# Performance work log

Hardware: AMD Instinct MI355X
Metric: run time of the kernel (lower is better)

Reference implementation:

```python
import jax, jax.numpy as jnp
import numpy as np

D = 256

def setup_inputs() -> dict:
    key = jax.random.key(0)
    k1, k2, k3, k4, k5, k6 = jax.random.split(key, 6)
    M, N = 2048, 512
    s = 1.0 / np.sqrt(D)
    return {
        "q_vec": jax.random.normal(k1, (M, D), dtype=jnp.float32),
        "kv": jax.random.normal(k2, (M, N, D), dtype=jnp.float32),
        "wq": jax.random.uniform(k3, (D, D), jnp.float32, -s, s),
        "wk": jax.random.uniform(k4, (D, D), jnp.float32, -s, s),
        "wv": jax.random.uniform(k5, (D, D), jnp.float32, -s, s),
        "wo": (jax.random.uniform(k6, (D, D), jnp.float32, -s, s)),
    }

def reference(q_vec, kv, wq, wk, wv, wo):
    # q_vec: [M, d], kv: [M, N, d]; weights stored torch-style [out, in] -> apply x @ W.T
    d = q_vec.shape[-1]
    q = q_vec @ wq.T                          # [M, d]
    k = jnp.einsum('mnd,ed->mne', kv, wk)     # [M, N, d]
    v = jnp.einsum('mnd,ed->mne', kv, wv)     # [M, N, d]
    logits = jnp.einsum('md,mnd->mn', q, k) / jnp.sqrt(jnp.float32(d))  # [M, N]
    attn = jax.nn.softmax(logits, axis=-1)    # [M, N] (dropout p=0.0 is identity)
    ctx = jnp.einsum('mn,mnd->md', attn, v)   # [M, d]
    out = ctx @ wo.T                          # [M, d]
    return out, attn
```

## Files before the change

### kernel.cpp

```cpp
#include <hip/hip_runtime.h>
#include <math.h>

#define DD 256
#define MM 2048
#define NN 512

typedef float f32x4 __attribute__((ext_vector_type(4)));

__device__ inline f32x4 ld_nt(const f32x4* p) {
    return __builtin_nontemporal_load(p);
}

__global__ void prep_weights(const float* __restrict__ wq, const float* __restrict__ wk,
                             const float* __restrict__ wv, const float* __restrict__ wo,
                             float* __restrict__ B1, float* __restrict__ B2T) {
    __shared__ float sA[DD];
    const int j = threadIdx.x;
    const int b = blockIdx.x;
    if (b < DD) {
        const int d = b;
        sA[j] = wq[j * DD + d];
        __syncthreads();
        float acc = 0.f;
        for (int a = 0; a < DD; ++a) acc = fmaf(sA[a], wk[a * DD + j], acc);
        B1[d * DD + j] = acc * 0.0625f;
    } else {
        const int d = b - DD;
        sA[j] = wv[j * DD + d];
        __syncthreads();
        float acc = 0.f;
        for (int e = 0; e < DD; ++e) acc = fmaf(wo[j * DD + e], sA[e], acc);
        B2T[d * DD + j] = acc;
    }
}

__global__ __launch_bounds__(256, 4)
void attn_fused(const float* __restrict__ q_vec, const float* __restrict__ kv,
                const float* __restrict__ B1, const float* __restrict__ B2T,
                float* __restrict__ out, float* __restrict__ attn_out) {
    __shared__ float s_pe[NN];
    __shared__ float s_lw[4];
    __shared__ float s_wc[4][DD];
    __shared__ float s_q[DD];
    __shared__ float s_qt[DD];

    const int m    = blockIdx.x;
    const int tid  = threadIdx.x;
    const int wave = tid >> 6;
    const int lane = tid & 63;
    const int grp  = lane >> 4;
    const int l16  = lane & 15;

    s_q[tid] = q_vec[(size_t)m * DD + tid];
    __syncthreads();
    {
        float a = 0.f;
#pragma unroll 8
        for (int d = 0; d < DD; ++d) a = fmaf(s_q[d], B1[d * DD + tid], a);
        s_qt[tid] = a;
    }
    __syncthreads();

    const f32x4* qt4 = (const f32x4*)s_qt;
    const f32x4 qv0 = qt4[l16];
    const f32x4 qv1 = qt4[l16 + 16];
    const f32x4 qv2 = qt4[l16 + 32];
    const f32x4 qv3 = qt4[l16 + 48];

    const int nbase = wave * 4 + grp;
    const f32x4* p = (const f32x4*)(kv + (size_t)m * NN * DD) + (size_t)nbase * 64 + l16;
    const int STRIDE = 16 * 64;

    f32x4 c0 = (f32x4)0.f, c1 = (f32x4)0.f, c2 = (f32x4)0.f, c3 = (f32x4)0.f;
    float lw = 0.f;

    f32x4 a0 = ld_nt(p), a1 = ld_nt(p + 16), a2 = ld_nt(p + 32), a3 = ld_nt(p + 48);

#pragma unroll 2
    for (int it = 0; it < NN / 16; ++it) {
        f32x4 b0, b1, b2, b3;
        if (it + 1 < NN / 16) {
            const f32x4* np = p + (size_t)(it + 1) * STRIDE;
            b0 = ld_nt(np); b1 = ld_nt(np + 16); b2 = ld_nt(np + 32); b3 = ld_nt(np + 48);
        }
        f32x4 t = a0 * qv0 + a1 * qv1 + a2 * qv2 + a3 * qv3;
        float pdot = (t[0] + t[1]) + (t[2] + t[3]);
        pdot += __shfl_xor(pdot, 1);
        pdot += __shfl_xor(pdot, 2);
        pdot += __shfl_xor(pdot, 4);
        pdot += __shfl_xor(pdot, 8);

        const float pe = __expf(pdot);
        if (l16 == 0) s_pe[it * 16 + nbase] = pe;
        lw += pe;

        c0 += pe * a0;
        c1 += pe * a1;
        c2 += pe * a2;
        c3 += pe * a3;

        a0 = b0; a1 = b1; a2 = b2; a3 = b3;
    }

#pragma unroll
    for (int i = 0; i < 4; ++i) {
        c0[i] += __shfl_xor(c0[i], 16); c1[i] += __shfl_xor(c1[i], 16);
        c2[i] += __shfl_xor(c2[i], 16); c3[i] += __shfl_xor(c3[i], 16);
        c0[i] += __shfl_xor(c0[i], 32); c1[i] += __shfl_xor(c1[i], 32);
        c2[i] += __shfl_xor(c2[i], 32); c3[i] += __shfl_xor(c3[i], 32);
    }
    lw += __shfl_xor(lw, 16);
    lw += __shfl_xor(lw, 32);

    {
        f32x4* wc4 = (f32x4*)(&s_wc[wave][0]);
        const f32x4 cg = (grp == 0) ? c0 : (grp == 1) ? c1 : (grp == 2) ? c2 : c3;
        wc4[grp * 16 + l16] = cg;
        if (lane == 0) s_lw[wave] = lw;
    }
    __syncthreads();

    const float L = s_lw[0] + s_lw[1] + s_lw[2] + s_lw[3];
    const float invL = 1.f / L;

    float cd = (s_wc[0][tid] + s_wc[1][tid]) + (s_wc[2][tid] + s_wc[3][tid]);
    cd *= invL;
    __syncthreads();
    s_q[tid] = cd;
    __syncthreads();

    attn_out[(size_t)m * NN + tid]       = s_pe[tid] * invL;
    attn_out[(size_t)m * NN + tid + 256] = s_pe[tid + 256] * invL;

    float o = 0.f;
#pragma unroll 8
    for (int d = 0; d < DD; ++d) o = fmaf(s_q[d], B2T[d * DD + tid], o);
    out[(size_t)m * DD + tid] = o;
}

extern "C" void kernel_launch(void* const* d_in, const int* in_sizes, int n_in,
                              void* d_out, int out_size, void* d_ws, size_t ws_size,
                              hipStream_t stream) {
    const float* q_vec = (const float*)d_in[0];
    const float* kv    = (const float*)d_in[1];
    const float* wq    = (const float*)d_in[2];
    const float* wk    = (const float*)d_in[3];
    const float* wv    = (const float*)d_in[4];
    const float* wo    = (const float*)d_in[5];

    float* out  = (float*)d_out;
    float* attn = (float*)d_out + (size_t)MM * DD;

    float* B1  = (float*)d_ws;
    float* B2T = B1 + DD * DD;

    prep_weights<<<2 * DD, DD, 0, stream>>>(wq, wk, wv, wo, B1, B2T);
    attn_fused<<<MM, DD, 0, stream>>>(q_vec, kv, B1, B2T, out, attn);
}
```

Baseline: 208.8 us.

## Process two query rows per block with deeper kv prefetch and shared weight reads

Each block now handles two rows of M, so every weight element read in the query projection and the output projection serves two rows. The kv streaming loop now runs across both rows with a two-stage register prefetch, and the first kv tiles are issued before the projection so memory latency overlaps it. The grid is halved to 1024 blocks, leaving fewer blocks to hide latency, and the extra prefetch registers may reduce occupancy.

Measured after the change: 467.8 us. 124% more time.

```diff
diff --git a/kernel.cpp b/kernel.cpp
--- a/kernel.cpp
+++ b/kernel.cpp
@@ -7,13 +7,11 @@
 
 typedef float f32x4 __attribute__((ext_vector_type(4)));
 
-__device__ inline f32x4 ld_nt(const f32x4* p) {
-    return __builtin_nontemporal_load(p);
-}
+__device__ inline f32x4 ld_nt(const f32x4* p) { return __builtin_nontemporal_load(p); }
 
 __global__ void prep_weights(const float* __restrict__ wq, const float* __restrict__ wk,
                              const float* __restrict__ wv, const float* __restrict__ wo,
-                             float* __restrict__ B1, float* __restrict__ B2T) {
+                             float* __restrict__ W1, float* __restrict__ W2T) {
     __shared__ float sA[DD];
     const int j = threadIdx.x;
     const int b = blockIdx.x;
@@ -23,119 +21,139 @@
         __syncthreads();
         float acc = 0.f;
         for (int a = 0; a < DD; ++a) acc = fmaf(sA[a], wk[a * DD + j], acc);
-        B1[d * DD + j] = acc * 0.0625f;
+        W1[d * DD + j] = acc * 0.0625f;
     } else {
         const int d = b - DD;
         sA[j] = wv[j * DD + d];
         __syncthreads();
         float acc = 0.f;
         for (int e = 0; e < DD; ++e) acc = fmaf(wo[j * DD + e], sA[e], acc);
-        B2T[d * DD + j] = acc;
+        W2T[d * DD + j] = acc;
     }
 }
 
 __global__ __launch_bounds__(256, 4)
 void attn_fused(const float* __restrict__ q_vec, const float* __restrict__ kv,
-                const float* __restrict__ B1, const float* __restrict__ B2T,
+                const float* __restrict__ W1, const float* __restrict__ W2T,
                 float* __restrict__ out, float* __restrict__ attn_out) {
     __shared__ float s_pe[NN];
     __shared__ float s_lw[4];
     __shared__ float s_wc[4][DD];
-    __shared__ float s_q[DD];
-    __shared__ float s_qt[DD];
+    __shared__ float s_qa[DD], s_qb[DD];
+    __shared__ float s_qt0[DD], s_qt1[DD];
 
-    const int m    = blockIdx.x;
+    const int m0   = blockIdx.x * 2;
     const int tid  = threadIdx.x;
     const int wave = tid >> 6;
     const int lane = tid & 63;
     const int grp  = lane >> 4;
     const int l16  = lane & 15;
+    const int nbase = wave * 4 + grp;
 
-    s_q[tid] = q_vec[(size_t)m * DD + tid];
+    const f32x4* kvb = (const f32x4*)(kv + (size_t)m0 * NN * DD);
+    const int lofs   = nbase * 64 + l16;
+    const int STRIDE = 16 * 64;
+    const int NT     = 2 * NN / 16;
+
+    f32x4 A0, A1, A2, A3, P0, P1, P2, P3;
+    {
+        const f32x4* p = kvb + lofs;
+        A0 = ld_nt(p); A1 = ld_nt(p + 16); A2 = ld_nt(p + 32); A3 = ld_nt(p + 48);
+        const f32x4* q = kvb + STRIDE + lofs;
+        P0 = ld_nt(q); P1 = ld_nt(q + 16); P2 = ld_nt(q + 32); P3 = ld_nt(q + 48);
+    }
+
+    s_qa[tid] = q_vec[(size_t)m0 * DD + tid];
+    s_qb[tid] = q_vec[(size_t)m0 * DD + DD + tid];
     __syncthreads();
     {
-        float a = 0.f;
+        float t0 = 0.f, t1 = 0.f;
 #pragma unroll 8
-        for (int d = 0; d < DD; ++d) a = fmaf(s_q[d], B1[d * DD + tid], a);
-        s_qt[tid] = a;
+        for (int d = 0; d < DD; ++d) {
+            const float w = W1[d * DD + tid];
+            t0 = fmaf(s_qa[d], w, t0);
+            t1 = fmaf(s_qb[d], w, t1);
+        }
+        s_qt0[tid] = t0;
+        s_qt1[tid] = t1;
     }
     __syncthreads();
 
-    const f32x4* qt4 = (const f32x4*)s_qt;
-    const f32x4 qv0 = qt4[l16];
-    const f32x4 qv1 = qt4[l16 + 16];
-    const f32x4 qv2 = qt4[l16 + 32];
-    const f32x4 qv3 = qt4[l16 + 48];
+    for (int r = 0; r < 2; ++r) {
+        const f32x4* qt4 = (const f32x4*)(r == 0 ? s_qt0 : s_qt1);
+        const f32x4 qv0 = qt4[l16];
+        const f32x4 qv1 = qt4[l16 + 16];
+        const f32x4 qv2 = qt4[l16 + 32];
+        const f32x4 qv3 = qt4[l16 + 48];
 
-    const int nbase = wave * 4 + grp;
-    const f32x4* p = (const f32x4*)(kv + (size_t)m * NN * DD) + (size_t)nbase * 64 + l16;
-    const int STRIDE = 16 * 64;
+        f32x4 c0 = (f32x4)0.f, c1 = (f32x4)0.f, c2 = (f32x4)0.f, c3 = (f32x4)0.f;
+        float lw = 0.f;
 
-    f32x4 c0 = (f32x4)0.f, c1 = (f32x4)0.f, c2 = (f32x4)0.f, c3 = (f32x4)0.f;
-    float lw = 0.f;
+        for (int it = 0; it < NN / 16; ++it) {
+            const int g = r * (NN / 16) + it;
+            f32x4 N0, N1, N2, N3;
+            const bool pf = (g + 2 < NT);
+            if (pf) {
+                const f32x4* np = kvb + (size_t)(g + 2) * STRIDE + lofs;
+                N0 = ld_nt(np); N1 = ld_nt(np + 16); N2 = ld_nt(np + 32); N3 = ld_nt(np + 48);
+            }
 
-    f32x4 a0 = ld_nt(p), a1 = ld_nt(p + 16), a2 = ld_nt(p + 32), a3 = ld_nt(p + 48);
+            f32x4 t = A0 * qv0 + A1 * qv1 + A2 * qv2 + A3 * qv3;
+            float pd = (t[0] + t[1]) + (t[2] + t[3]);
+            pd += __shfl_xor(pd, 1);
+            pd += __shfl_xor(pd, 2);
+            pd += __shfl_xor(pd, 4);
+            pd += __shfl_xor(pd, 8);
 
-#pragma unroll 2
-    for (int it = 0; it < NN / 16; ++it) {
-        f32x4 b0, b1, b2, b3;
-        if (it + 1 < NN / 16) {
-            const f32x4* np = p + (size_t)(it + 1) * STRIDE;
-            b0 = ld_nt(np); b1 = ld_nt(np + 16); b2 = ld_nt(np + 32); b3 = ld_nt(np + 48);
+            const float pe = __expf(pd);
+            if (l16 == 0) s_pe[it * 16 + nbase] = pe;
+            lw += pe;
+
+            c0 += pe * A0; c1 += pe * A1; c2 += pe * A2; c3 += pe * A3;
+
+            A0 = P0; A1 = P1; A2 = P2; A3 = P3;
+            if (pf) { P0 = N0; P1 = N1; P2 = N2; P3 = N3; }
         }
-        f32x4 t = a0 * qv0 + a1 * qv1 + a2 * qv2 + a3 * qv3;
-        float pdot = (t[0] + t[1]) + (t[2] + t[3]);
-        pdot += __shfl_xor(pdot, 1);
-        pdot += __shfl_xor(pdot, 2);
-        pdot += __shfl_xor(pdot, 4);
-        pdot += __shfl_xor(pdot, 8);
 
-        const float pe = __expf(pdot);
-        if (l16 == 0) s_pe[it * 16 + nbase] = pe;
-        lw += pe;
+#pragma unroll
+        for (int i = 0; i < 4; ++i) {
+            c0[i] += __shfl_xor(c0[i], 16); c1[i] += __shfl_xor(c1[i], 16);
+            c2[i] += __shfl_xor(c2[i], 16); c3[i] += __shfl_xor(c3[i], 16);
+            c0[i] += __shfl_xor(c0[i], 32); c1[i] += __shfl_xor(c1[i], 32);
+            c2[i] += __shfl_xor(c2[i], 32); c3[i] += __shfl_xor(c3[i], 32);
+        }
+        lw += __shfl_xor(lw, 16);
+        lw += __shfl_xor(lw, 32);
 
-        c0 += pe * a0;
-        c1 += pe * a1;
-        c2 += pe * a2;
-        c3 += pe * a3;
+        {
+            f32x4* wc4 = (f32x4*)(&s_wc[wave][0]);
+            const f32x4 cg = (grp == 0) ? c0 : (grp == 1) ? c1 : (grp == 2) ? c2 : c3;
+            wc4[grp * 16 + l16] = cg;
+            if (lane == 0) s_lw[wave] = lw;
+        }
+        __syncthreads();
 
-        a0 = b0; a1 = b1; a2 = b2; a3 = b3;
+        const float L = (s_lw[0] + s_lw[1]) + (s_lw[2] + s_lw[3]);
+        const float invL = 1.f / L;
+        const float cd = ((s_wc[0][tid] + s_wc[1][tid]) + (s_wc[2][tid] + s_wc[3][tid])) * invL;
+
+        if (r == 0) s_qa[tid] = cd; else s_qb[tid] = cd;
+        attn_out[(size_t)(m0 + r) * NN + tid]       = s_pe[tid] * invL;
+        attn_out[(size_t)(m0 + r) * NN + tid + 256] = s_pe[tid + 256] * invL;
+        __syncthreads();
     }
 
-#pragma unroll
-    for (int i = 0; i < 4; ++i) {
-        c0[i] += __shfl_xor(c0[i], 16); c1[i] += __shfl_xor(c1[i], 16);
-        c2[i] += __shfl_xor(c2[i], 16); c3[i] += __shfl_xor(c3[i], 16);
-        c0[i] += __shfl_xor(c0[i], 32); c1[i] += __shfl_xor(c1[i], 32);
-        c2[i] += __shfl_xor(c2[i], 32); c3[i] += __shfl_xor(c3[i], 32);
+    {
+        float o0 = 0.f, o1 = 0.f;
+#pragma unroll 8
+        for (int d = 0; d < DD; ++d) {
+            const float w = W2T[d * DD + tid];
+            o0 = fmaf(s_qa[d], w, o0);
+            o1 = fmaf(s_qb[d], w, o1);
+        }
+        out[(size_t)m0 * DD + tid]      = o0;
+        out[(size_t)m0 * DD + DD + tid] = o1;
     }
-    lw += __shfl_xor(lw, 16);
-    lw += __shfl_xor(lw, 32);
-
-    {
-        f32x4* wc4 = (f32x4*)(&s_wc[wave][0]);
-        const f32x4 cg = (grp == 0) ? c0 : (grp == 1) ? c1 : (grp == 2) ? c2 : c3;
-        wc4[grp * 16 + l16] = cg;
-        if (lane == 0) s_lw[wave] = lw;
-    }
-    __syncthreads();
-
-    const float L = s_lw[0] + s_lw[1] + s_lw[2] + s_lw[3];
-    const float invL = 1.f / L;
-
-    float cd = (s_wc[0][tid] + s_wc[1][tid]) + (s_wc[2][tid] + s_wc[3][tid]);
-    cd *= invL;
-    __syncthreads();
-    s_q[tid] = cd;
-    __syncthreads();
-
-    attn_out[(size_t)m * NN + tid]       = s_pe[tid] * invL;
-    attn_out[(size_t)m * NN + tid + 256] = s_pe[tid + 256] * invL;
-
-    float o = 0.f;
-#pragma unroll 8
-    for (int d = 0; d < DD; ++d) o = fmaf(s_q[d], B2T[d * DD + tid], o);
-    out[(size_t)m * DD + tid] = o;
 }
 
 extern "C" void kernel_launch(void* const* d_in, const int* in_sizes, int n_in,
@@ -151,9 +169,9 @@
     float* out  = (float*)d_out;
     float* attn = (float*)d_out + (size_t)MM * DD;
 
-    float* B1  = (float*)d_ws;
-    float* B2T = B1 + DD * DD;
+    float* W1  = (float*)d_ws;
+    float* W2T = W1 + DD * DD;
 
-    prep_weights<<<2 * DD, DD, 0, stream>>>(wq, wk, wv, wo, B1, B2T);
-    attn_fused<<<MM, DD, 0, stream>>>(q_vec, kv, B1, B2T, out, attn);
+    prep_weights<<<2 * DD, DD, 0, stream>>>(wq, wk, wv, wo, W1, W2T);
+    attn_fused<<<MM / 2, DD, 0, stream>>>(q_vec, kv, W1, W2T, out, attn);
 }
```

## Split per-row q and output projections into batched row-GEMM kernels

Applied to the files above, without the earlier changes.

Moves the q·W1 and ctx·W2T matrix-vector products out of the streaming attention kernel into separate 16-row GEMM kernels, so each weight row load is reused across 16 rows instead of being reloaded by every block. The attention kernel now only streams kv, and it issues the first kv loads before reading qt so global latency overlaps the setup. This adds two kernel launches and round-trips qt and ctx through workspace memory.

New measurement: 229.0 us. 1.1x slower.

```diff
diff --git a/kernel.cpp b/kernel.cpp
--- a/kernel.cpp
+++ b/kernel.cpp
@@ -7,13 +7,11 @@
 
 typedef float f32x4 __attribute__((ext_vector_type(4)));
 
-__device__ inline f32x4 ld_nt(const f32x4* p) {
-    return __builtin_nontemporal_load(p);
-}
+__device__ inline f32x4 ld_nt(const f32x4* p) { return __builtin_nontemporal_load(p); }
 
 __global__ void prep_weights(const float* __restrict__ wq, const float* __restrict__ wk,
                              const float* __restrict__ wv, const float* __restrict__ wo,
-                             float* __restrict__ B1, float* __restrict__ B2T) {
+                             float* __restrict__ W1, float* __restrict__ W2T) {
     __shared__ float sA[DD];
     const int j = threadIdx.x;
     const int b = blockIdx.x;
@@ -23,25 +21,42 @@
         __syncthreads();
         float acc = 0.f;
         for (int a = 0; a < DD; ++a) acc = fmaf(sA[a], wk[a * DD + j], acc);
-        B1[d * DD + j] = acc * 0.0625f;
+        W1[d * DD + j] = acc * 0.0625f;
     } else {
         const int d = b - DD;
         sA[j] = wv[j * DD + d];
         __syncthreads();
         float acc = 0.f;
         for (int e = 0; e < DD; ++e) acc = fmaf(wo[j * DD + e], sA[e], acc);
-        B2T[d * DD + j] = acc;
+        W2T[d * DD + j] = acc;
     }
 }
 
+template <int ROWS>
+__global__ void rowgemm(const float* __restrict__ X, const float* __restrict__ W,
+                        float* __restrict__ Y) {
+    __shared__ float sX[ROWS][DD];
+    const int j = threadIdx.x;
+    const int m0 = blockIdx.x * ROWS;
+    for (int r = 0; r < ROWS; ++r) sX[r][j] = X[(size_t)(m0 + r) * DD + j];
+    __syncthreads();
+    float acc[ROWS];
+#pragma unroll
+    for (int r = 0; r < ROWS; ++r) acc[r] = 0.f;
+    for (int d = 0; d < DD; ++d) {
+        const float w = W[d * DD + j];
+#pragma unroll
+        for (int r = 0; r < ROWS; ++r) acc[r] = fmaf(sX[r][d], w, acc[r]);
+    }
+    for (int r = 0; r < ROWS; ++r) Y[(size_t)(m0 + r) * DD + j] = acc[r];
+}
+
 __global__ __launch_bounds__(256, 4)
-void attn_fused(const float* __restrict__ q_vec, const float* __restrict__ kv,
-                const float* __restrict__ B1, const float* __restrict__ B2T,
-                float* __restrict__ out, float* __restrict__ attn_out) {
+void attn_stream(const float* __restrict__ kv, const float* __restrict__ qt,
+                 float* __restrict__ c_out, float* __restrict__ attn_out) {
     __shared__ float s_pe[NN];
     __shared__ float s_lw[4];
     __shared__ float s_wc[4][DD];
-    __shared__ float s_q[DD];
     __shared__ float s_qt[DD];
 
     const int m    = blockIdx.x;
@@ -50,15 +65,14 @@
     const int lane = tid & 63;
     const int grp  = lane >> 4;
     const int l16  = lane & 15;
+    const int nbase = wave * 4 + grp;
 
-    s_q[tid] = q_vec[(size_t)m * DD + tid];
-    __syncthreads();
-    {
-        float a = 0.f;
-#pragma unroll 8
-        for (int d = 0; d < DD; ++d) a = fmaf(s_q[d], B1[d * DD + tid], a);
-        s_qt[tid] = a;
-    }
+    const f32x4* p = (const f32x4*)(kv + (size_t)m * NN * DD) + (size_t)nbase * 64 + l16;
+    const int STRIDE = 16 * 64;
+
+    f32x4 a0 = ld_nt(p), a1 = ld_nt(p + 16), a2 = ld_nt(p + 32), a3 = ld_nt(p + 48);
+
+    s_qt[tid] = qt[(size_t)m * DD + tid];
     __syncthreads();
 
     const f32x4* qt4 = (const f32x4*)s_qt;
@@ -67,14 +81,8 @@
     const f32x4 qv2 = qt4[l16 + 32];
     const f32x4 qv3 = qt4[l16 + 48];
 
-    const int nbase = wave * 4 + grp;
-    const f32x4* p = (const f32x4*)(kv + (size_t)m * NN * DD) + (size_t)nbase * 64 + l16;
-    const int STRIDE = 16 * 64;
-
     f32x4 c0 = (f32x4)0.f, c1 = (f32x4)0.f, c2 = (f32x4)0.f, c3 = (f32x4)0.f;
     float lw = 0.f;
-
-    f32x4 a0 = ld_nt(p), a1 = ld_nt(p + 16), a2 = ld_nt(p + 32), a3 = ld_nt(p + 48);
 
 #pragma unroll 2
     for (int it = 0; it < NN / 16; ++it) {
@@ -84,13 +92,13 @@
             b0 = ld_nt(np); b1 = ld_nt(np + 16); b2 = ld_nt(np + 32); b3 = ld_nt(np + 48);
         }
         f32x4 t = a0 * qv0 + a1 * qv1 + a2 * qv2 + a3 * qv3;
-        float pdot = (t[0] + t[1]) + (t[2] + t[3]);
-        pdot += __shfl_xor(pdot, 1);
-        pdot += __shfl_xor(pdot, 2);
-        pdot += __shfl_xor(pdot, 4);
-        pdot += __shfl_xor(pdot, 8);
+        float pd = (t[0] + t[1]) + (t[2] + t[3]);
+        pd += __shfl_xor(pd, 1);
+        pd += __shfl_xor(pd, 2);
+        pd += __shfl_xor(pd, 4);
+        pd += __shfl_xor(pd, 8);
 
-        const float pe = __expf(pdot);
+        const float pe = __expf(pd);
         if (l16 == 0) s_pe[it * 16 + nbase] = pe;
         lw += pe;
 
@@ -120,22 +128,14 @@
     }
     __syncthreads();
 
-    const float L = s_lw[0] + s_lw[1] + s_lw[2] + s_lw[3];
+    const float L = (s_lw[0] + s_lw[1]) + (s_lw[2] + s_lw[3]);
     const float invL = 1.f / L;
 
-    float cd = (s_wc[0][tid] + s_wc[1][tid]) + (s_wc[2][tid] + s_wc[3][tid]);
-    cd *= invL;
-    __syncthreads();
-    s_q[tid] = cd;
-    __syncthreads();
+    const float cd = ((s_wc[0][tid] + s_wc[1][tid]) + (s_wc[2][tid] + s_wc[3][tid])) * invL;
+    c_out[(size_t)m * DD + tid] = cd;
 
     attn_out[(size_t)m * NN + tid]       = s_pe[tid] * invL;
     attn_out[(size_t)m * NN + tid + 256] = s_pe[tid + 256] * invL;
-
-    float o = 0.f;
-#pragma unroll 8
-    for (int d = 0; d < DD; ++d) o = fmaf(s_q[d], B2T[d * DD + tid], o);
-    out[(size_t)m * DD + tid] = o;
 }
 
 extern "C" void kernel_launch(void* const* d_in, const int* in_sizes, int n_in,
@@ -151,9 +151,13 @@
     float* out  = (float*)d_out;
     float* attn = (float*)d_out + (size_t)MM * DD;
 
-    float* B1  = (float*)d_ws;
-    float* B2T = B1 + DD * DD;
+    float* W1  = (float*)d_ws;
+    float* W2T = W1 + DD * DD;
+    float* qt  = W2T + DD * DD;
+    float* cws = qt + (size_t)MM * DD;
 
-    prep_weights<<<2 * DD, DD, 0, stream>>>(wq, wk, wv, wo, B1, B2T);
-    attn_fused<<<MM, DD, 0, stream>>>(q_vec, kv, B1, B2T, out, attn);
+    prep_weights<<<2 * DD, DD, 0, stream>>>(wq, wk, wv, wo, W1, W2T);
+    rowgemm<16><<<MM / 16, DD, 0, stream>>>(q_vec, W1, qt);
+    attn_stream<<<MM, DD, 0, stream>>>(kv, qt, cws, attn);
+    rowgemm<16><<<MM / 16, DD, 0, stream>>>(cws, W2T, out);
 }
```
